# Optimization experiments

Measured on AMD Instinct MI355X. Metric: run time of the kernel, lower is better.

Reference implementation:

```python
import jax, jax.numpy as jnp
import numpy as np

EPS = 1e-5
NEG_SLOPE = 0.01  # F.leaky_relu default

N0, N1, N2 = 100000, 25000, 5000
E0, E1 = 800000, 160000
D_IN, D_HID, D_OUT = 256, 256, 128


def setup_inputs() -> dict:
    key = jax.random.key(0)
    ks = jax.random.split(key, 16)
    inp = {
        "x": jax.random.normal(ks[0], (N0, D_IN), dtype=jnp.float32),
        "src0": jax.random.randint(ks[1], (E0,), 0, N0, dtype=jnp.int32),
        "dst0": jax.random.randint(ks[2], (E0,), 0, N1, dtype=jnp.int32),
        "val0": jnp.arange(E0, dtype=jnp.int32),
        "src1": jax.random.randint(ks[3], (E1,), 0, N1, dtype=jnp.int32),
        "dst1": jax.random.randint(ks[4], (E1,), 0, N2, dtype=jnp.int32),
        "val1": jnp.arange(E1, dtype=jnp.int32),
        "timestamps": jax.random.randint(ks[5], (E0 + E1,), 0, 100, dtype=jnp.int32),
        "time": 50,
        "interval": 10,
        # SAGEConv layer 1 (in -> hidden): lin_l (bias) on aggregated, lin_r (no bias) on root
        "W1l": jax.random.normal(ks[6], (D_IN, D_HID), dtype=jnp.float32) / np.sqrt(D_IN),
        "W1r": jax.random.normal(ks[7], (D_IN, D_HID), dtype=jnp.float32) / np.sqrt(D_IN),
        "b1": jnp.zeros((D_HID,), dtype=jnp.float32),
        # BatchNorm1d params (eval mode: running stats)
        "g1": jnp.ones((D_HID,), dtype=jnp.float32),
        "bt1": jnp.zeros((D_HID,), dtype=jnp.float32),
        "rm1": jax.random.normal(ks[8], (D_HID,), dtype=jnp.float32) * 0.1,
        "rv1": jax.random.uniform(ks[9], (D_HID,), dtype=jnp.float32) + 0.5,
        # SAGEConv layer 2 (hidden -> out)
        "W2l": jax.random.normal(ks[10], (D_HID, D_OUT), dtype=jnp.float32) / np.sqrt(D_HID),
        "W2r": jax.random.normal(ks[11], (D_HID, D_OUT), dtype=jnp.float32) / np.sqrt(D_HID),
        "b2": jnp.zeros((D_OUT,), dtype=jnp.float32),
    }
    return inp


def _time_mask(val, timestamps, time, interval):
    # time_sparse keeps edges whose timestamp is in {time, ..., time+interval-1}
    ts = timestamps[val]
    return (ts >= time) & (ts < time + interval)


def _sage_conv(x_src, x_tgt, src, dst, mask, Wl, Wr, b, n_tgt):
    m = mask.astype(x_src.dtype)
    msg = x_src[src] * m[:, None]               # [E, D] gather + mask
    agg = jax.ops.segment_sum(msg, dst, num_segments=n_tgt)
    deg = jax.ops.segment_sum(m, dst, num_segments=n_tgt)
    agg = agg / jnp.maximum(deg, 1.0)[:, None]  # mean aggregation
    return agg @ Wl + b + x_tgt @ Wr


def reference(x, src0, dst0, val0, src1, dst1, val1, timestamps, time, interval,
              W1l, W1r, b1, g1, bt1, rm1, rv1, W2l, W2r, b2):
    # layer 0: N0 -> N1
    mask0 = _time_mask(val0, timestamps, time, interval)
    h = _sage_conv(x, x[:N1], src0, dst0, mask0, W1l, W1r, b1, N1)
    # BatchNorm1d (eval) + leaky_relu; dropout is identity in eval
    h = (h - rm1) * jax.lax.rsqrt(rv1 + EPS) * g1 + bt1
    h = jnp.where(h >= 0, h, NEG_SLOPE * h)
    # layer 1: N1 -> N2
    mask1 = _time_mask(val1, timestamps, time, interval)
    out = _sage_conv(h, h[:N2], src1, dst1, mask1, W2l, W2r, b2, N2)
    return out, mask1
```

## Files before the change

kernel.cpp:

```cpp
#include <hip/hip_runtime.h>

#define N1c 25000
#define N2c 5000
#define Dc 256
#define DOUTc 128
#define EPSc 1e-5f
#define NEGc 0.01f
#define CAPc 32

typedef __attribute__((ext_vector_type(8))) short short8;
typedef __attribute__((ext_vector_type(4))) float f32x4;

__device__ __forceinline__ ushort f2bf(float f) {
    unsigned u = __float_as_uint(f);
    u += 0x7fffu + ((u >> 16) & 1u);
    return (ushort)(u >> 16);
}
__device__ __forceinline__ float bf2f(ushort u) {
    return __uint_as_float(((unsigned)u) << 16);
}
__device__ __forceinline__ int imin(int a, int b) { return a < b ? a : b; }
__device__ __forceinline__ int imax(int a, int b) { return a > b ? a : b; }

__global__ __launch_bounds__(256) void prep_fill(
    const int* __restrict__ src0, const int* __restrict__ dst0, const int* __restrict__ val0,
    const int* __restrict__ src1, const int* __restrict__ dst1, const int* __restrict__ val1,
    const int* __restrict__ ts, const int* __restrict__ time_p, const int* __restrict__ itv_p,
    const float* __restrict__ W1l, const float* __restrict__ W1r,
    const float* __restrict__ W2l, const float* __restrict__ W2r,
    int E0, int E1,
    ushort* __restrict__ Bt1, ushort* __restrict__ Bt2,
    int* __restrict__ cnt0, int* __restrict__ cnt1,
    int* __restrict__ eidx0, int* __restrict__ eidx1,
    float* __restrict__ mask_out) {
    const int flat = blockIdx.x * blockDim.x + threadIdx.x;
    const int NT = gridDim.x * blockDim.x;
    const int t0 = *time_p, iv = *itv_p;

    __shared__ float tl[32][33];
    const int tx = threadIdx.x & 31, ty = threadIdx.x >> 5;
    for (int t = blockIdx.x; t < 192; t += gridDim.x) {
        const bool L1 = t < 128;
        const int tt = L1 ? t : t - 128;
        const int ntn = L1 ? 8 : 4;
        const int kt = tt / ntn, nt = tt % ntn;
        const int k0 = kt * 32, n0 = nt * 32;
        const float* Wl = L1 ? W1l : W2l;
        const float* Wr = L1 ? W1r : W2r;
        const int nst = L1 ? 256 : 128;
        ushort* Bt = L1 ? Bt1 : Bt2;
#pragma unroll
        for (int rr = 0; rr < 4; ++rr) {
            int r = ty * 4 + rr;
            int k = k0 + r;
            tl[r][tx] = (k < 256) ? Wl[(size_t)k * nst + n0 + tx]
                                  : Wr[(size_t)(k - 256) * nst + n0 + tx];
        }
        __syncthreads();
#pragma unroll
        for (int rr = 0; rr < 4; ++rr) {
            int r = ty * 4 + rr;
            Bt[(size_t)(n0 + r) * 512 + k0 + tx] = f2bf(tl[tx][r]);
        }
        __syncthreads();
    }

    for (int e = flat; e < E0; e += NT) {
        int t = ts[val0[e]];
        if (t >= t0 && t < t0 + iv) {
            int d = dst0[e];
            int pos = atomicAdd(&cnt0[d], 1);
            if (pos < CAPc) eidx0[d * CAPc + pos] = src0[e];
        }
    }
    for (int e = flat; e < E1; e += NT) {
        int t = ts[val1[e]];
        bool m = (t >= t0 && t < t0 + iv);
        mask_out[e] = m ? 1.0f : 0.0f;
        if (m) {
            int d = dst1[e];
            int pos = atomicAdd(&cnt1[d], 1);
            if (pos < CAPc) eidx1[d * CAPc + pos] = src1[e];
        }
    }
}

template <int VARIANT, int BMT, int NJW>
__global__ __launch_bounds__(256, 4) void fused_gemm(
    const void* __restrict__ Asrc,
    const int* __restrict__ cnt, const int* __restrict__ eidx,
    const int* __restrict__ src, const int* __restrict__ dst,
    const int* __restrict__ val, const int* __restrict__ ts,
    const int* __restrict__ time_p, const int* __restrict__ itv_p, int E,
    const ushort* __restrict__ Bt,
    const float* __restrict__ bias,
    const float* __restrict__ g, const float* __restrict__ bt,
    const float* __restrict__ rm, const float* __restrict__ rv,
    void* __restrict__ Cout, int M) {
    constexpr int RT = BMT / 16;
    constexpr int RPW = BMT / 4;
    __shared__ ushort As[BMT][536];
    const int tid = threadIdx.x;
    const int wave = tid >> 6, lane = tid & 63;
    const int quad = lane >> 4, l16 = lane & 15;
    const int m0 = blockIdx.x * BMT;
    const float* Xf = (const float*)Asrc;
    const ushort* Hb = (const ushort*)Asrc;

    int ms_[RPW], cs_[RPW], my_[RPW];
#pragma unroll
    for (int i = 0; i < RPW; ++i) {
        ms_[i] = m0 + wave * RPW + i;
        cs_[i] = (ms_[i] < M) ? cnt[ms_[i]] : 0;
    }
#pragma unroll
    for (int i = 0; i < RPW; ++i)
        my_[i] = (ms_[i] < M && lane < CAPc) ? eidx[ms_[i] * CAPc + lane] : 0;
#pragma unroll
    for (int i = 0; i < RPW; ++i) {
        int r = wave * RPW + i;
        int mm = imax(0, imin(ms_[i], M - 1));
        if (VARIANT == 0) {
            float4 rt = *(const float4*)(Xf + (size_t)mm * Dc + lane * 4);
            ushort4 ro;
            ro.x = f2bf(rt.x); ro.y = f2bf(rt.y); ro.z = f2bf(rt.z); ro.w = f2bf(rt.w);
            *(ushort4*)&As[r][256 + lane * 4] = (ms_[i] < M) ? ro : make_ushort4(0, 0, 0, 0);
        } else {
            ushort4 rb = *(const ushort4*)(Hb + (size_t)mm * Dc + lane * 4);
            *(ushort4*)&As[r][256 + lane * 4] = (ms_[i] < M) ? rb : make_ushort4(0, 0, 0, 0);
        }
    }
#pragma unroll
    for (int i = 0; i < RPW; ++i)
        my_[i] = (lane < cs_[i]) ? my_[i] : 0;

    float4 acc_[RPW];
#pragma unroll
    for (int i = 0; i < RPW; ++i) acc_[i] = make_float4(0.f, 0.f, 0.f, 0.f);

#pragma unroll
    for (int p = 0; p < RPW; p += 2) {
        float4 vf[2][4];
        ushort4 vb[2][4];
        int ccs[2];
#pragma unroll
        for (int q = 0; q < 2; ++q) {
            int cc = imin(cs_[p + q], CAPc);
            ccs[q] = cc;
#pragma unroll
            for (int u = 0; u < 4; ++u) {
                int e = imax(0, imin(u, cc - 1));
                int s = __shfl(my_[p + q], e, 64);
                if (VARIANT == 0) vf[q][u] = *(const float4*)(Xf + (size_t)s * Dc + lane * 4);
                else              vb[q][u] = *(const ushort4*)(Hb + (size_t)s * Dc + lane * 4);
            }
        }
#pragma unroll
        for (int q = 0; q < 2; ++q) {
            int i = p + q;
            int cc = ccs[q];
#pragma unroll
            for (int u = 0; u < 4; ++u) {
                if (u < cc) {
                    if (VARIANT == 0) {
                        acc_[i].x += vf[q][u].x; acc_[i].y += vf[q][u].y;
                        acc_[i].z += vf[q][u].z; acc_[i].w += vf[q][u].w;
                    } else {
                        acc_[i].x += bf2f(vb[q][u].x); acc_[i].y += bf2f(vb[q][u].y);
                        acc_[i].z += bf2f(vb[q][u].z); acc_[i].w += bf2f(vb[q][u].w);
                    }
                }
            }
            for (int jb = 4; jb < cc; jb += 4) {
#pragma unroll
                for (int u = 0; u < 4; ++u) {
                    int e = imin(jb + u, cc - 1);
                    int s = __shfl(my_[i], e, 64);
                    if (jb + u < cc) {
                        if (VARIANT == 0) {
                            float4 v = *(const float4*)(Xf + (size_t)s * Dc + lane * 4);
                            acc_[i].x += v.x; acc_[i].y += v.y; acc_[i].z += v.z; acc_[i].w += v.w;
                        } else {
                            ushort4 v = *(const ushort4*)(Hb + (size_t)s * Dc + lane * 4);
                            acc_[i].x += bf2f(v.x); acc_[i].y += bf2f(v.y);
                            acc_[i].z += bf2f(v.z); acc_[i].w += bf2f(v.w);
                        }
                    }
                }
            }
        }
    }
#pragma unroll
    for (int i = 0; i < RPW; ++i) {
        if (cs_[i] > CAPc) {
            float4 a = make_float4(0.f, 0.f, 0.f, 0.f);
            int t0 = *time_p, iv = *itv_p;
            for (int e = 0; e < E; ++e) {
                if (dst[e] != ms_[i]) continue;
                int t = ts[val[e]];
                if (t >= t0 && t < t0 + iv) {
                    if (VARIANT == 0) {
                        float4 v = *(const float4*)(Xf + (size_t)src[e] * Dc + lane * 4);
                        a.x += v.x; a.y += v.y; a.z += v.z; a.w += v.w;
                    } else {
                        ushort4 v = *(const ushort4*)(Hb + (size_t)src[e] * Dc + lane * 4);
                        a.x += bf2f(v.x); a.y += bf2f(v.y); a.z += bf2f(v.z); a.w += bf2f(v.w);
                    }
                }
            }
            acc_[i] = a;
        }
    }
#pragma unroll
    for (int i = 0; i < RPW; ++i) {
        int r = wave * RPW + i;
        if (ms_[i] >= M) {
            *(ushort4*)&As[r][lane * 4] = make_ushort4(0, 0, 0, 0);
            continue;
        }
        float inv = 1.0f / fmaxf((float)cs_[i], 1.0f);
        ushort4 o;
        o.x = f2bf(acc_[i].x * inv); o.y = f2bf(acc_[i].y * inv);
        o.z = f2bf(acc_[i].z * inv); o.w = f2bf(acc_[i].w * inv);
        *(ushort4*)&As[r][lane * 4] = o;
    }
    __syncthreads();

    f32x4 acc[RT][NJW] = {};
    const ushort* Bw = Bt + (size_t)((wave * NJW) * 16 + l16) * 512 + quad * 8;
    for (int k0 = 0; k0 < 512; k0 += 32) {
        short8 af[RT];
#pragma unroll
        for (int rt = 0; rt < RT; ++rt)
            af[rt] = *(const short8*)&As[rt * 16 + l16][k0 + quad * 8];
        uint4 bfr[NJW];
#pragma unroll
        for (int jj = 0; jj < NJW; ++jj)
            bfr[jj] = *(const uint4*)(Bw + (size_t)jj * 16 * 512 + k0);
#pragma unroll
        for (int jj = 0; jj < NJW; ++jj) {
            short8 bf = *reinterpret_cast<const short8*>(&bfr[jj]);
#pragma unroll
            for (int rt = 0; rt < RT; ++rt)
                acc[rt][jj] = __builtin_amdgcn_mfma_f32_16x16x32_bf16(af[rt], bf, acc[rt][jj], 0, 0, 0);
        }
    }

#pragma unroll
    for (int jj = 0; jj < NJW; ++jj) {
        int gn = (wave * NJW + jj) * 16 + l16;
        float sc = 1.f, sh = bias[gn];
        if (VARIANT == 0) {
            float s = g[gn] * rsqrtf(rv[gn] + EPSc);
            sh = (bias[gn] - rm[gn]) * s + bt[gn];
            sc = s;
        }
#pragma unroll
        for (int rt = 0; rt < RT; ++rt) {
            int gmb = m0 + rt * 16 + quad * 4;
#pragma unroll
            for (int rr = 0; rr < 4; ++rr) {
                int gm = gmb + rr;
                if (gm >= M) continue;
                float v = acc[rt][jj][rr];
                if (VARIANT == 0) {
                    v = v * sc + sh;
                    v = v >= 0.f ? v : NEGc * v;
                    ((ushort*)Cout)[(size_t)gm * Dc + gn] = f2bf(v);
                } else {
                    ((float*)Cout)[(size_t)gm * DOUTc + gn] = v + sh;
                }
            }
        }
    }
}

extern "C" void kernel_launch(void* const* d_in, const int* in_sizes, int n_in,
                              void* d_out, int out_size, void* d_ws, size_t ws_size,
                              hipStream_t stream) {
    const float* x    = (const float*)d_in[0];
    const int* src0   = (const int*)d_in[1];
    const int* dst0   = (const int*)d_in[2];
    const int* val0   = (const int*)d_in[3];
    const int* src1   = (const int*)d_in[4];
    const int* dst1   = (const int*)d_in[5];
    const int* val1   = (const int*)d_in[6];
    const int* ts     = (const int*)d_in[7];
    const int* time_p = (const int*)d_in[8];
    const int* itv_p  = (const int*)d_in[9];
    const float* W1l  = (const float*)d_in[10];
    const float* W1r  = (const float*)d_in[11];
    const float* b1   = (const float*)d_in[12];
    const float* g1   = (const float*)d_in[13];
    const float* bt1  = (const float*)d_in[14];
    const float* rm1  = (const float*)d_in[15];
    const float* rv1  = (const float*)d_in[16];
    const float* W2l  = (const float*)d_in[17];
    const float* W2r  = (const float*)d_in[18];
    const float* b2   = (const float*)d_in[19];
    int E0 = in_sizes[1];
    int E1 = in_sizes[4];
    float* out = (float*)d_out;

    ushort* h    = (ushort*)d_ws;
    ushort* Bt1  = h    + (size_t)N1c * Dc;
    ushort* Bt2  = Bt1  + 256 * 512;
    int* ip      = (int*)(Bt2 + 128 * 512);
    int* cnt0    = ip;             ip += N1c;
    int* cnt1    = ip;             ip += N2c;
    int* eidx0   = ip;             ip += N1c * CAPc;
    int* eidx1   = ip;             ip += N2c * CAPc;
    float* mask_tail = out + (size_t)N2c * DOUTc;

    hipMemsetAsync(cnt0, 0, (size_t)(N1c + N2c) * sizeof(int), stream);

    prep_fill<<<2048, 256, 0, stream>>>(
        src0, dst0, val0, src1, dst1, val1, ts, time_p, itv_p,
        W1l, W1r, W2l, W2r, E0, E1, Bt1, Bt2,
        cnt0, cnt1, eidx0, eidx1, mask_tail);
    fused_gemm<0, 32, 4><<<(N1c + 31) / 32, 256, 0, stream>>>(
        x, cnt0, eidx0, src0, dst0, val0, ts, time_p, itv_p, E0,
        Bt1, b1, g1, bt1, rm1, rv1, h, N1c);
    fused_gemm<1, 16, 2><<<(N2c + 15) / 16, 256, 0, stream>>>(
        h, cnt1, eidx1, src1, dst1, val1, ts, time_p, itv_p, E1,
        Bt2, b2, nullptr, nullptr, nullptr, nullptr, out, N2c);
}
```

Baseline: 252.4 us.

## Double-buffer neighbor gathers across row pairs and relax launch bounds

```diff
diff --git a/kernel.cpp b/kernel.cpp
--- a/kernel.cpp
+++ b/kernel.cpp
@@ -86,7 +86,7 @@
 }
 
 template <int VARIANT, int BMT, int NJW>
-__global__ __launch_bounds__(256, 4) void fused_gemm(
+__global__ __launch_bounds__(256, 2) void fused_gemm(
     const void* __restrict__ Asrc,
     const int* __restrict__ cnt, const int* __restrict__ eidx,
     const int* __restrict__ src, const int* __restrict__ dst,
@@ -99,6 +99,7 @@
     void* __restrict__ Cout, int M) {
     constexpr int RT = BMT / 16;
     constexpr int RPW = BMT / 4;
+    static_assert(RPW == 4 || RPW == 8, "pipeline written for RPW 4/8");
     __shared__ ushort As[BMT][536];
     const int tid = threadIdx.x;
     const int wave = tid >> 6, lane = tid & 63;
@@ -138,15 +139,13 @@
 #pragma unroll
     for (int i = 0; i < RPW; ++i) acc_[i] = make_float4(0.f, 0.f, 0.f, 0.f);
 
-#pragma unroll
-    for (int p = 0; p < RPW; p += 2) {
-        float4 vf[2][4];
-        ushort4 vb[2][4];
-        int ccs[2];
+    float4 fA[2][4], fB[2][4];
+    ushort4 bA[2][4], bB[2][4];
+
+    auto ISSUE = [&](int p, float4 (&vf)[2][4], ushort4 (&vb)[2][4]) {
 #pragma unroll
         for (int q = 0; q < 2; ++q) {
             int cc = imin(cs_[p + q], CAPc);
-            ccs[q] = cc;
 #pragma unroll
             for (int u = 0; u < 4; ++u) {
                 int e = imax(0, imin(u, cc - 1));
@@ -155,10 +154,12 @@
                 else              vb[q][u] = *(const ushort4*)(Hb + (size_t)s * Dc + lane * 4);
             }
         }
+    };
+    auto ACCUM = [&](int p, float4 (&vf)[2][4], ushort4 (&vb)[2][4]) {
 #pragma unroll
         for (int q = 0; q < 2; ++q) {
             int i = p + q;
-            int cc = ccs[q];
+            int cc = imin(cs_[i], CAPc);
 #pragma unroll
             for (int u = 0; u < 4; ++u) {
                 if (u < cc) {
@@ -189,7 +190,26 @@
                 }
             }
         }
-    }
+    };
+
+    ISSUE(0, fA, bA);
+    __builtin_amdgcn_sched_barrier(0);
+    ISSUE(2, fB, bB);
+    __builtin_amdgcn_sched_barrier(0);
+    if constexpr (RPW == 8) {
+        ACCUM(0, fA, bA);
+        ISSUE(4, fA, bA);
+        __builtin_amdgcn_sched_barrier(0);
+        ACCUM(2, fB, bB);
+        ISSUE(6, fB, bB);
+        __builtin_amdgcn_sched_barrier(0);
+        ACCUM(4, fA, bA);
+        ACCUM(6, fB, bB);
+    } else {
+        ACCUM(0, fA, bA);
+        ACCUM(2, fB, bB);
+    }
+
 #pragma unroll
     for (int i = 0; i < RPW; ++i) {
         if (cs_[i] > CAPc) {
```

New measurement: 250.2 us. About the same (-0.9%).
